# Kernel tuning notes

Hardware: AMD Instinct MI355X
Metric: run time of the kernel (lower is better)

The kernel has to match this reference:

```python
import jax, jax.numpy as jnp
import numpy as np

EPS = 1e-6      # torch F.pairwise_distance default eps (added to the difference)
MARGIN = 1.0

def _cdist_eps(a, b):
    # Exact ||a_i - b_j + eps||_2 via expansion:
    # ||a-b+eps||^2 = ||a||^2 + ||b||^2 - 2 a.b + 2*eps*(sum(a)-sum(b)) + D*eps^2
    D = a.shape[-1]
    sq = (jnp.sum(a * a, axis=1)[:, None]
          + jnp.sum(b * b, axis=1)[None, :]
          - 2.0 * (a @ b.T)
          + 2.0 * EPS * (jnp.sum(a, axis=1)[:, None] - jnp.sum(b, axis=1)[None, :])
          + D * EPS * EPS)
    return jnp.sqrt(jnp.maximum(sq, 0.0))

def setup_inputs() -> dict:
    key = jax.random.key(0)
    k1, k2, k3 = jax.random.split(key, 3)
    B, D = 4096, 1024
    return {
        'anchor_embeddings': jax.random.normal(k1, (B, D), dtype=jnp.float32),
        'positive_embeddings': jax.random.normal(k2, (B, D), dtype=jnp.float32),
        'negative_embeddings': jax.random.normal(k3, (B, D), dtype=jnp.float32),
    }

def reference(anchor_embeddings, positive_embeddings, negative_embeddings):
    a, p, n = anchor_embeddings, positive_embeddings, negative_embeddings
    # per-row anchor-positive and anchor-negative distances
    d_ap = jnp.linalg.norm(a - p + EPS, axis=-1)          # [B]
    d_an_row = jnp.linalg.norm(a - n + EPS, axis=-1)      # [B]

    # hardest negative: for each anchor, max over negatives with dist < d_ap[i], else 0
    dan_mat = _cdist_eps(a, n)                            # [B, B]
    mask_n = dan_mat < d_ap[:, None]
    hard_n = jnp.where(mask_n.any(axis=1),
                       jnp.max(jnp.where(mask_n, dan_mat, -jnp.inf), axis=1),
                       0.0)
    d_an = jnp.mean(hard_n)                               # scalar

    # hardest positive: for each anchor, min over positives with dist > d(a_i, n_i), else 0
    dpp_mat = _cdist_eps(a, p)                            # [B, B]
    mask_p = dpp_mat > d_an_row[:, None]
    hard_p = jnp.where(mask_p.any(axis=1),
                       jnp.min(jnp.where(mask_p, dpp_mat, jnp.inf), axis=1),
                       0.0)
    d_pp = jnp.mean(hard_p)                               # scalar

    loss = jnp.mean(jnp.clip(d_ap - 0.5 * d_pp - 0.5 * d_an + MARGIN, 0.0, None))
    return loss
```

## Files before the change

kernel.cpp:

```cpp
#include <hip/hip_runtime.h>


#define NB 4096
#define DIM 1024
#define EPSF 1e-6f
#define D_EPS2 (1024.0f * 1e-6f * 1e-6f)

#define BM 256
#define BN 128
#define BK 64

typedef __bf16  bf16x8 __attribute__((ext_vector_type(8)));
typedef float   f32x4  __attribute__((ext_vector_type(4)));

__device__ __forceinline__ unsigned short f2bf(float x) {
    unsigned u = __float_as_uint(x);
    u += 0x7FFFu + ((u >> 16) & 1u);
    return (unsigned short)(u >> 16);
}

__device__ __forceinline__ void g2l16(const unsigned short* g, unsigned short* l) {
    __builtin_amdgcn_global_load_lds(
        (const __attribute__((address_space(1))) unsigned int*)g,
        (__attribute__((address_space(3))) unsigned int*)l, 16, 0, 0);
}


__global__ __launch_bounds__(256) void row_stats_kernel(
    const float* __restrict__ a, const float* __restrict__ p,
    const float* __restrict__ n,
    unsigned short* __restrict__ abf, unsigned short* __restrict__ pbf,
    unsigned short* __restrict__ nbf, float* __restrict__ stats)
{
    const int t    = threadIdx.x;
    const int wave = t >> 6, lane = t & 63;
    const int row  = blockIdx.x * 4 + wave;
    const size_t base = (size_t)row * DIM;

    const float4* a4 = (const float4*)(a + base);
    const float4* p4 = (const float4*)(p + base);
    const float4* n4 = (const float4*)(n + base);

    float v[8] = {0,0,0,0,0,0,0,0};
#pragma unroll
    for (int c = 0; c < 4; c++) {
        const int idx = c * 64 + lane;
        const float4 va = a4[idx];
        const float4 vp = p4[idx];
        const float4 vn = n4[idx];
        const float fa[4] = {va.x, va.y, va.z, va.w};
        const float fp[4] = {vp.x, vp.y, vp.z, vp.w};
        const float fn[4] = {vn.x, vn.y, vn.z, vn.w};
#pragma unroll
        for (int e = 0; e < 4; e++) {
            v[0] += fa[e];           v[1] += fa[e] * fa[e];
            v[2] += fp[e];           v[3] += fp[e] * fp[e];
            v[4] += fn[e];           v[5] += fn[e] * fn[e];
            float dp = fa[e] - fp[e] + EPSF;  v[6] += dp * dp;
            float dn = fa[e] - fn[e] + EPSF;  v[7] += dn * dn;
        }
        ushort4 ba, bp, bn;
        ba.x = f2bf(fa[0]); ba.y = f2bf(fa[1]); ba.z = f2bf(fa[2]); ba.w = f2bf(fa[3]);
        bp.x = f2bf(fp[0]); bp.y = f2bf(fp[1]); bp.z = f2bf(fp[2]); bp.w = f2bf(fp[3]);
        bn.x = f2bf(fn[0]); bn.y = f2bf(fn[1]); bn.z = f2bf(fn[2]); bn.w = f2bf(fn[3]);
        ((ushort4*)(abf + base))[idx] = ba;
        ((ushort4*)(pbf + base))[idx] = bp;
        ((ushort4*)(nbf + base))[idx] = bn;
    }

#pragma unroll
    for (int m = 32; m >= 1; m >>= 1)
#pragma unroll
        for (int q = 0; q < 8; q++) v[q] += __shfl_xor(v[q], m);

    if (lane == 0) {
        stats[0 * NB + row] = v[1] + 2.0f * EPSF * v[0] + D_EPS2;
        stats[1 * NB + row] = v[5] - 2.0f * EPSF * v[4];
        stats[2 * NB + row] = v[3] - 2.0f * EPSF * v[2];
        stats[3 * NB + row] = sqrtf(v[6]);
        stats[4 * NB + row] = sqrtf(v[7]);
        ((unsigned*)stats)[5 * NB + row] = 0u;
        ((unsigned*)stats)[6 * NB + row] = 0x7f800000u;
    }
}

__global__ __launch_bounds__(512, 2) void gemm_mask_kernel(
    const unsigned short* __restrict__ Abf,
    const unsigned short* __restrict__ Nbf,
    const unsigned short* __restrict__ Pbf,
    float* __restrict__ stats)
{
    const int i0 = blockIdx.x * BM;
    const int j0 = blockIdx.y * BN;

    __shared__ unsigned short sA[2][BM * BK];
    __shared__ unsigned short sN[2][BN * BK];
    __shared__ unsigned short sP[2][BN * BK];

    const int t    = threadIdx.x;
    const int wave = t >> 6, lane = t & 63;
    const int wm   = wave >> 1, wn = wave & 1;
    const int quad = lane >> 4, lrow = lane & 15;

    const int srow = t >> 3;
    const int slot = t & 7;
    const int kch  = (slot ^ (srow & 7)) * 8;
    const unsigned short* gA = Abf + (size_t)(i0 + srow) * DIM + kch;
    const unsigned short* gN = Nbf + (size_t)(j0 + srow) * DIM + kch;
    const unsigned short* gP = Pbf + (size_t)(j0 + srow) * DIM + kch;
    const int lofs = srow * BK + slot * 8;

    const int aoff = (wm * 64 + lrow) * BK;
    const int boff = (wn * 64 + lrow) * BK;
    const int rk0  = ((0 + quad) ^ (lrow & 7)) * 8;
    const int rk1  = ((4 + quad) ^ (lrow & 7)) * 8;

    f32x4 accN[4][4], accP[4][4];
#pragma unroll
    for (int im = 0; im < 4; im++)
#pragma unroll
        for (int jn = 0; jn < 4; jn++) {
            accN[im][jn] = (f32x4)(0.0f);
            accP[im][jn] = (f32x4)(0.0f);
        }

#define STAGE_A(NBUF, KTN)                                                    \
    _Pragma("unroll")                                                         \
    for (int g = 0; g < 4; g++)                                               \
        g2l16(gA + (size_t)(KTN) + (size_t)(g * 64) * DIM,                    \
              &sA[NBUF][(g * 64) * BK + lofs]);

#define STAGE_NP(NBUF, KTN)                                                   \
    _Pragma("unroll")                                                         \
    for (int g = 0; g < 2; g++) {                                             \
        g2l16(gN + (size_t)(KTN) + (size_t)(g * 64) * DIM,                    \
              &sN[NBUF][(g * 64) * BK + lofs]);                               \
        g2l16(gP + (size_t)(KTN) + (size_t)(g * 64) * DIM,                    \
              &sP[NBUF][(g * 64) * BK + lofs]);                               \
    }

#define MFMA16(ACC, AF, BF)                                                   \
    _Pragma("unroll")                                                         \
    for (int im = 0; im < 4; im++)                                            \
        _Pragma("unroll")                                                     \
        for (int jn = 0; jn < 4; jn++)                                        \
            ACC[im][jn] = __builtin_amdgcn_mfma_f32_16x16x32_bf16(            \
                AF[im], BF[jn], ACC[im][jn], 0, 0, 0);

#define TILE(B, NBUF, KTN, DO_STAGE)                                          \
  {                                                                           \
    bf16x8 af0[4], af1[4], bfr[4];                                            \
                                       \
    _Pragma("unroll")                                                         \
    for (int im = 0; im < 4; im++)                                            \
        af0[im] = *(const bf16x8*)&sA[B][aoff + im * 16 * BK + rk0];          \
    _Pragma("unroll")                                                         \
    for (int jn = 0; jn < 4; jn++)                                            \
        bfr[jn] = *(const bf16x8*)&sN[B][boff + jn * 16 * BK + rk0];          \
    if (DO_STAGE) { STAGE_A(NBUF, KTN); }                                     \
    __builtin_amdgcn_s_barrier();                                             \
    asm volatile("s_waitcnt lgkmcnt(0)" ::: "memory");                        \
    __builtin_amdgcn_s_setprio(1);                                            \
    MFMA16(accN, af0, bfr);                                                   \
    __builtin_amdgcn_s_setprio(0);                                            \
    __builtin_amdgcn_s_barrier();                                             \
                                     \
    _Pragma("unroll")                                                         \
    for (int im = 0; im < 4; im++)                                            \
        af1[im] = *(const bf16x8*)&sA[B][aoff + im * 16 * BK + rk1];          \
    _Pragma("unroll")                                                         \
    for (int jn = 0; jn < 4; jn++)                                            \
        bfr[jn] = *(const bf16x8*)&sN[B][boff + jn * 16 * BK + rk1];          \
    if (DO_STAGE) { STAGE_NP(NBUF, KTN); }                                    \
    __builtin_amdgcn_s_barrier();                                             \
    asm volatile("s_waitcnt lgkmcnt(0)" ::: "memory");                        \
    __builtin_amdgcn_s_setprio(1);                                            \
    MFMA16(accN, af1, bfr);                                                   \
    __builtin_amdgcn_s_setprio(0);                                            \
    __builtin_amdgcn_s_barrier();                                             \
                                                      \
    _Pragma("unroll")                                                         \
    for (int jn = 0; jn < 4; jn++)                                            \
        bfr[jn] = *(const bf16x8*)&sP[B][boff + jn * 16 * BK + rk0];          \
    __builtin_amdgcn_s_barrier();                                             \
    asm volatile("s_waitcnt lgkmcnt(0)" ::: "memory");                        \
    __builtin_amdgcn_s_setprio(1);                                            \
    MFMA16(accP, af0, bfr);                                                   \
    __builtin_amdgcn_s_setprio(0);                                            \
    __builtin_amdgcn_s_barrier();                                             \
         \
    _Pragma("unroll")                                                         \
    for (int jn = 0; jn < 4; jn++)                                            \
        bfr[jn] = *(const bf16x8*)&sP[B][boff + jn * 16 * BK + rk1];          \
    __builtin_amdgcn_s_barrier();                                             \
    asm volatile("s_waitcnt lgkmcnt(0)" ::: "memory");                        \
    __builtin_amdgcn_s_setprio(1);                                            \
    MFMA16(accP, af1, bfr);                                                   \
    __builtin_amdgcn_s_setprio(0);                                            \
    asm volatile("s_waitcnt vmcnt(0)" ::: "memory");                          \
    __builtin_amdgcn_s_barrier();                                             \
  }

    STAGE_A(0, 0);
    STAGE_NP(0, 0);
    asm volatile("s_waitcnt vmcnt(0)" ::: "memory");
    __builtin_amdgcn_s_barrier();

#pragma unroll 1
    for (int kt = 0; kt < DIM; kt += 2 * BK) {
        TILE(0, 1, kt + BK, 1);
        TILE(1, 0, kt + 2 * BK, (kt + 2 * BK) < DIM);
    }

#undef TILE
#undef MFMA16
#undef STAGE_NP
#undef STAGE_A

    const float* __restrict__ base_a = stats + 0 * NB;
    const float* __restrict__ cn_v   = stats + 1 * NB;
    const float* __restrict__ cp_v   = stats + 2 * NB;
    const float* __restrict__ d_ap   = stats + 3 * NB;
    const float* __restrict__ d_an   = stats + 4 * NB;
    unsigned* __restrict__ hard_n = ((unsigned*)stats) + 5 * NB;
    unsigned* __restrict__ hard_p = ((unsigned*)stats) + 6 * NB;

#pragma unroll
    for (int im = 0; im < 4; im++) {
#pragma unroll
        for (int r = 0; r < 4; r++) {
            const int gi = i0 + wm * 64 + im * 16 + quad * 4 + r;
            const float cutN = d_ap[gi];
            const float cutP = d_an[gi];
            const float bi   = base_a[gi];
            float bestN = 0.0f;
            float bestP = __uint_as_float(0x7f800000u);
#pragma unroll
            for (int jn = 0; jn < 4; jn++) {
                const int gj = j0 + wn * 64 + jn * 16 + lrow;
                const float dN = sqrtf(fmaxf(bi + cn_v[gj] - 2.0f * accN[im][jn][r], 0.0f));
                const float dP = sqrtf(fmaxf(bi + cp_v[gj] - 2.0f * accP[im][jn][r], 0.0f));
                if (dN < cutN && dN > bestN) bestN = dN;
                if (dP > cutP && dP < bestP) bestP = dP;
            }
#pragma unroll
            for (int m = 1; m < 16; m <<= 1) {
                bestN = fmaxf(bestN, __shfl_xor(bestN, m));
                bestP = fminf(bestP, __shfl_xor(bestP, m));
            }
            if (lrow == 0) {
                const unsigned bn_ = __float_as_uint(bestN);
                const unsigned bp_ = __float_as_uint(bestP);
                if (bn_ != 0u)          atomicMax(hard_n + gi, bn_);
                if (bp_ != 0x7f800000u) atomicMin(hard_p + gi, bp_);
            }
        }
    }
}

__global__ __launch_bounds__(1024) void finalize_kernel(
    const float* __restrict__ stats, float* __restrict__ out)
{
    const unsigned* hard_n = ((const unsigned*)stats) + 5 * NB;
    const unsigned* hard_p = ((const unsigned*)stats) + 6 * NB;
    const float*    d_ap   = stats + 3 * NB;
    const int t = threadIdx.x;
    const int wave = t >> 6, lane = t & 63;
    __shared__ float pn[16], pp[16];
    __shared__ float s_dan, s_dpp;

    float sn = 0.0f, sp = 0.0f;
    for (int i = t; i < NB; i += 1024) {
        sn += __uint_as_float(hard_n[i]);
        const unsigned hp = hard_p[i];
        if (hp != 0x7f800000u) sp += __uint_as_float(hp);
    }
#pragma unroll
    for (int m = 32; m >= 1; m >>= 1) {
        sn += __shfl_xor(sn, m);
        sp += __shfl_xor(sp, m);
    }
    if (lane == 0) { pn[wave] = sn; pp[wave] = sp; }
    __syncthreads();
    if (t == 0) {
        float an = 0.0f, ap = 0.0f;
#pragma unroll
        for (int w = 0; w < 16; w++) { an += pn[w]; ap += pp[w]; }
        s_dan = an / (float)NB;
        s_dpp = ap / (float)NB;
    }
    __syncthreads();
    const float dan = s_dan, dpp = s_dpp;

    float accv = 0.0f;
    for (int i = t; i < NB; i += 1024)
        accv += fmaxf(d_ap[i] - 0.5f * dpp - 0.5f * dan + 1.0f, 0.0f);
#pragma unroll
    for (int m = 32; m >= 1; m >>= 1) accv += __shfl_xor(accv, m);
    if (lane == 0) pn[wave] = accv;
    __syncthreads();
    if (t == 0) {
        float s = 0.0f;
#pragma unroll
        for (int w = 0; w < 16; w++) s += pn[w];
        out[0] = s / (float)NB;
    }
}

extern "C" void kernel_launch(void* const* d_in, const int* in_sizes, int n_in,
                              void* d_out, int out_size, void* d_ws, size_t ws_size,
                              hipStream_t stream) {
    const float* a = (const float*)d_in[0];
    const float* p = (const float*)d_in[1];
    const float* n = (const float*)d_in[2];
    float* out = (float*)d_out;

    unsigned short* abf = (unsigned short*)d_ws;
    unsigned short* pbf = abf + (size_t)NB * DIM;
    unsigned short* nbf = pbf + (size_t)NB * DIM;
    float* stats = (float*)(nbf + (size_t)NB * DIM);

    row_stats_kernel<<<NB / 4, 256, 0, stream>>>(a, p, n, abf, pbf, nbf, stats);

    dim3 grid(NB / BM, NB / BN);
    gemm_mask_kernel<<<grid, 512, 0, stream>>>(abf, nbf, pbf, stats);

    finalize_kernel<<<1, 1024, 0, stream>>>(stats, out);
}
```

Before: 184.7 us.

## Stagger N/P tile staging and use partial vmcnt waits in GEMM main loop

Restructures the double-buffered K loop so the N and P next-tile loads are issued in separate phases, with P staged later. The end-of-tile full vmcnt(0) wait becomes partial vmcnt(6)/vmcnt(2) waits, keeping more global-to-LDS loads in flight behind the MFMAs. The last tile is peeled out of the loop to drop the conditional staging. This adds tricky wait-count accounting that must exactly match how many loads are outstanding to stay correct.

```diff
diff --git a/kernel.cpp b/kernel.cpp
--- a/kernel.cpp
+++ b/kernel.cpp
@@ -130,14 +130,32 @@
         g2l16(gA + (size_t)(KTN) + (size_t)(g * 64) * DIM,                    \
               &sA[NBUF][(g * 64) * BK + lofs]);
 
-#define STAGE_NP(NBUF, KTN)                                                   \
-    _Pragma("unroll")                                                         \
-    for (int g = 0; g < 2; g++) {                                             \
+#define STAGE_N(NBUF, KTN)                                                    \
+    _Pragma("unroll")                                                         \
+    for (int g = 0; g < 2; g++)                                               \
         g2l16(gN + (size_t)(KTN) + (size_t)(g * 64) * DIM,                    \
-              &sN[NBUF][(g * 64) * BK + lofs]);                               \
+              &sN[NBUF][(g * 64) * BK + lofs]);
+
+#define STAGE_P(NBUF, KTN)                                                    \
+    _Pragma("unroll")                                                         \
+    for (int g = 0; g < 2; g++)                                               \
         g2l16(gP + (size_t)(KTN) + (size_t)(g * 64) * DIM,                    \
-              &sP[NBUF][(g * 64) * BK + lofs]);                               \
-    }
+              &sP[NBUF][(g * 64) * BK + lofs]);
+
+#define LOAD_AF(DST, BUF, RK)                                                 \
+    _Pragma("unroll")                                                         \
+    for (int im = 0; im < 4; im++)                                            \
+        DST[im] = *(const bf16x8*)&sA[BUF][aoff + im * 16 * BK + (RK)];
+
+#define LOAD_NF(DST, BUF, RK)                                                 \
+    _Pragma("unroll")                                                         \
+    for (int jn = 0; jn < 4; jn++)                                            \
+        DST[jn] = *(const bf16x8*)&sN[BUF][boff + jn * 16 * BK + (RK)];
+
+#define LOAD_PF(DST, BUF, RK)                                                 \
+    _Pragma("unroll")                                                         \
+    for (int jn = 0; jn < 4; jn++)                                            \
+        DST[jn] = *(const bf16x8*)&sP[BUF][boff + jn * 16 * BK + (RK)];
 
 #define MFMA16(ACC, AF, BF)                                                   \
     _Pragma("unroll")                                                         \
@@ -147,74 +165,81 @@
             ACC[im][jn] = __builtin_amdgcn_mfma_f32_16x16x32_bf16(            \
                 AF[im], BF[jn], ACC[im][jn], 0, 0, 0);
 
-#define TILE(B, NBUF, KTN, DO_STAGE)                                          \
-  {                                                                           \
-    bf16x8 af0[4], af1[4], bfr[4];                                            \
-                                       \
-    _Pragma("unroll")                                                         \
-    for (int im = 0; im < 4; im++)                                            \
-        af0[im] = *(const bf16x8*)&sA[B][aoff + im * 16 * BK + rk0];          \
-    _Pragma("unroll")                                                         \
-    for (int jn = 0; jn < 4; jn++)                                            \
-        bfr[jn] = *(const bf16x8*)&sN[B][boff + jn * 16 * BK + rk0];          \
-    if (DO_STAGE) { STAGE_A(NBUF, KTN); }                                     \
-    __builtin_amdgcn_s_barrier();                                             \
-    asm volatile("s_waitcnt lgkmcnt(0)" ::: "memory");                        \
-    __builtin_amdgcn_s_setprio(1);                                            \
-    MFMA16(accN, af0, bfr);                                                   \
-    __builtin_amdgcn_s_setprio(0);                                            \
-    __builtin_amdgcn_s_barrier();                                             \
-                                     \
-    _Pragma("unroll")                                                         \
-    for (int im = 0; im < 4; im++)                                            \
-        af1[im] = *(const bf16x8*)&sA[B][aoff + im * 16 * BK + rk1];          \
-    _Pragma("unroll")                                                         \
-    for (int jn = 0; jn < 4; jn++)                                            \
-        bfr[jn] = *(const bf16x8*)&sN[B][boff + jn * 16 * BK + rk1];          \
-    if (DO_STAGE) { STAGE_NP(NBUF, KTN); }                                    \
-    __builtin_amdgcn_s_barrier();                                             \
-    asm volatile("s_waitcnt lgkmcnt(0)" ::: "memory");                        \
-    __builtin_amdgcn_s_setprio(1);                                            \
-    MFMA16(accN, af1, bfr);                                                   \
-    __builtin_amdgcn_s_setprio(0);                                            \
-    __builtin_amdgcn_s_barrier();                                             \
-                                                      \
-    _Pragma("unroll")                                                         \
-    for (int jn = 0; jn < 4; jn++)                                            \
-        bfr[jn] = *(const bf16x8*)&sP[B][boff + jn * 16 * BK + rk0];          \
-    __builtin_amdgcn_s_barrier();                                             \
-    asm volatile("s_waitcnt lgkmcnt(0)" ::: "memory");                        \
-    __builtin_amdgcn_s_setprio(1);                                            \
-    MFMA16(accP, af0, bfr);                                                   \
-    __builtin_amdgcn_s_setprio(0);                                            \
-    __builtin_amdgcn_s_barrier();                                             \
-         \
-    _Pragma("unroll")                                                         \
-    for (int jn = 0; jn < 4; jn++)                                            \
-        bfr[jn] = *(const bf16x8*)&sP[B][boff + jn * 16 * BK + rk1];          \
-    __builtin_amdgcn_s_barrier();                                             \
-    asm volatile("s_waitcnt lgkmcnt(0)" ::: "memory");                        \
-    __builtin_amdgcn_s_setprio(1);                                            \
-    MFMA16(accP, af1, bfr);                                                   \
-    __builtin_amdgcn_s_setprio(0);                                            \
-    asm volatile("s_waitcnt vmcnt(0)" ::: "memory");                          \
-    __builtin_amdgcn_s_barrier();                                             \
-  }
+#define BAR()    __builtin_amdgcn_s_barrier()
+#define LGKM0()  asm volatile("s_waitcnt lgkmcnt(0)" ::: "memory")
+#define PRIO(x)  __builtin_amdgcn_s_setprio(x)
 
     STAGE_A(0, 0);
-    STAGE_NP(0, 0);
+    STAGE_N(0, 0);
+    STAGE_P(0, 0);
     asm volatile("s_waitcnt vmcnt(0)" ::: "memory");
-    __builtin_amdgcn_s_barrier();
+    BAR();
 
 #pragma unroll 1
-    for (int kt = 0; kt < DIM; kt += 2 * BK) {
-        TILE(0, 1, kt + BK, 1);
-        TILE(1, 0, kt + 2 * BK, (kt + 2 * BK) < DIM);
-    }
-
-#undef TILE
+    for (int t15 = 0; t15 < 15; ++t15) {
+        const int cur = t15 & 1, nxt = cur ^ 1;
+        const int kn  = (t15 + 1) * BK;
+        bf16x8 af0[4], af1[4], bfr[4];
+        LOAD_AF(af0, cur, rk0);
+        LOAD_NF(bfr, cur, rk0);
+        STAGE_A(nxt, kn);
+        BAR(); LGKM0(); PRIO(1);
+        MFMA16(accN, af0, bfr);
+        PRIO(0); BAR();
+        LOAD_AF(af1, cur, rk1);
+        LOAD_NF(bfr, cur, rk1);
+        STAGE_N(nxt, kn);
+        BAR(); LGKM0(); PRIO(1);
+        MFMA16(accN, af1, bfr);
+        PRIO(0);
+        asm volatile("s_waitcnt vmcnt(6)" ::: "memory");
+        BAR();
+        LOAD_PF(bfr, cur, rk0);
+        STAGE_P(nxt, kn);
+        BAR(); LGKM0(); PRIO(1);
+        MFMA16(accP, af0, bfr);
+        PRIO(0); BAR();
+        LOAD_PF(bfr, cur, rk1);
+        BAR(); LGKM0(); PRIO(1);
+        MFMA16(accP, af1, bfr);
+        PRIO(0);
+        asm volatile("s_waitcnt vmcnt(2)" ::: "memory");
+        BAR();
+    }
+
+    {
+        bf16x8 af0[4], af1[4], bfr[4];
+        LOAD_AF(af0, 1, rk0);
+        LOAD_NF(bfr, 1, rk0);
+        BAR(); LGKM0(); PRIO(1);
+        MFMA16(accN, af0, bfr);
+        PRIO(0); BAR();
+        LOAD_AF(af1, 1, rk1);
+        LOAD_NF(bfr, 1, rk1);
+        BAR(); LGKM0(); PRIO(1);
+        MFMA16(accN, af1, bfr);
+        PRIO(0);
+        asm volatile("s_waitcnt vmcnt(0)" ::: "memory");
+        BAR();
+        LOAD_PF(bfr, 1, rk0);
+        BAR(); LGKM0(); PRIO(1);
+        MFMA16(accP, af0, bfr);
+        PRIO(0); BAR();
+        LOAD_PF(bfr, 1, rk1);
+        BAR(); LGKM0(); PRIO(1);
+        MFMA16(accP, af1, bfr);
+        PRIO(0);
+    }
+
+#undef BAR
+#undef LGKM0
+#undef PRIO
 #undef MFMA16
-#undef STAGE_NP
+#undef LOAD_PF
+#undef LOAD_NF
+#undef LOAD_AF
+#undef STAGE_P
+#undef STAGE_N
 #undef STAGE_A
 
     const float* __restrict__ base_a = stats + 0 * NB;
```

New measurement: 187.2 us. Within noise of the previous version (+1.3%).
